# Optimization experiments

Hardware: AMD Instinct MI355X
Metric: run time of the kernel (lower is better)

The kernel has to match this reference:

```python
import jax, jax.numpy as jnp
import numpy as np

B, T, E, H, N_TAGS = 128, 512, 256, 512, 32
START, END = 30, 31


def setup_inputs() -> dict:
    key = jax.random.key(0)
    ks = jax.random.split(key, 12)
    s = 1.0 / np.sqrt(H)

    def w(k, shape):
        return jax.random.normal(k, shape, jnp.float32) * s

    X = jax.random.normal(ks[0], (B, T, E), jnp.float32)
    length = jnp.sort(jax.random.randint(ks[1], (B,), T // 2, T + 1))[::-1]
    masks = (jnp.arange(T)[None, :] < length[:, None]).astype(jnp.float32)
    W_ih_f, W_hh_f, b_f = w(ks[2], (4 * H, E)), w(ks[3], (4 * H, H)), w(ks[4], (4 * H,))
    W_ih_b, W_hh_b, b_b = w(ks[5], (4 * H, E)), w(ks[6], (4 * H, H)), w(ks[7], (4 * H,))
    W_out, b_out = w(ks[8], (N_TAGS, 2 * H)), w(ks[9], (N_TAGS,))
    transitions = jax.random.normal(ks[10], (N_TAGS, N_TAGS), jnp.float32)
    transitions = transitions.at[:, START].set(-1e4).at[END, :].set(-1e4)
    return dict(X=X, masks=masks, length=length,
                W_ih_f=W_ih_f, W_hh_f=W_hh_f, b_f=b_f,
                W_ih_b=W_ih_b, W_hh_b=W_hh_b, b_b=b_b,
                W_out=W_out, b_out=b_out, transitions=transitions)


def _lstm_dir(Xt, mt, Wih, Whh, b, reverse):
    # Xt: [T,B,E], mt: [T,B,1]. Masked update emulates pack_padded_sequence
    # (state frozen on pad; for reverse dir, state stays zero until last valid token).
    h0 = jnp.zeros((Xt.shape[1], H), Xt.dtype)

    def step(carry, inp):
        h, c = carry
        x, m = inp
        gates = x @ Wih.T + h @ Whh.T + b  # [B,4H], torch gate order i,f,g,o
        i, f, g, o = jnp.split(gates, 4, axis=-1)
        i, f, o = jax.nn.sigmoid(i), jax.nn.sigmoid(f), jax.nn.sigmoid(o)
        g = jnp.tanh(g)
        c_new = f * c + i * g
        h_new = o * jnp.tanh(c_new)
        h = m * h_new + (1.0 - m) * h
        c = m * c_new + (1.0 - m) * c
        return (h, c), h

    _, hs = jax.lax.scan(step, (h0, h0), (Xt, mt), reverse=reverse)
    return hs  # [T,B,H]


def reference(X, masks, length, W_ih_f, W_hh_f, b_f, W_ih_b, W_hh_b, b_b, W_out, b_out, transitions):
    Xt = X.transpose(1, 0, 2)            # [T,B,E]
    mT = masks.T                          # [T,B]
    mt = mT[:, :, None]
    hf = _lstm_dir(Xt, mt, W_ih_f, W_hh_f, b_f, False)
    hb = _lstm_dir(Xt, mt, W_ih_b, W_hh_b, b_b, True)
    emis = jnp.concatenate([hf, hb], axis=-1) @ W_out.T + b_out  # [T,B,n_tags]

    # Viterbi forward recurrence with masking
    alphas0 = emis[0] + transitions[START]  # [B,n]

    def vstep(alphas, inp):
        e, m = inp  # e: [B,n], m: [B,1]
        scores = alphas[:, :, None] + transitions[None] + e[:, None, :]  # [B,from,to]
        alphas = m * scores.max(axis=1) + (1.0 - m) * alphas
        return alphas, jnp.argmax(scores, axis=1)

    alphas, bps = jax.lax.scan(vstep, alphas0, (emis[1:], mt[1:]))
    final = alphas + transitions[:, END]
    max_end_scores = final.max(axis=1)      # [B]
    end_tags = jnp.argmax(final, axis=1)    # [B]

    # Masked backtrace: bps[k] is the backpointer into position k+1
    def bstep(cur, inp):
        bp, m = inp  # bp: [B,n], m: [B]
        prev = jnp.where(m > 0, jnp.take_along_axis(bp, cur[:, None], axis=1)[:, 0], cur)
        return prev, prev

    _, outs = jax.lax.scan(bstep, end_tags, (bps, mT[1:]), reverse=True)  # outs[k]=tag at pos k
    tags = jnp.concatenate([outs, end_tags[None]], axis=0).T              # [B,T]
    tags = jnp.where(masks > 0, tags, -1)
    return max_end_scores, tags
```

## Files before the change

kernel.cpp:

```cpp
#include <hip/hip_runtime.h>
#include <cfloat>
#include <cmath>

#define Bn 128
#define Tn 512
#define En 256
#define Hn 512
#define NTAGS 32
#define CHK 64
#define NCHK 12

#define OFF_HF 0
#define OFF_HB 131072
#define OFF_CF 262144
#define OFF_CB 327680
#define OFF_EF 393216
#define OFF_EB 2490368

__device__ __forceinline__ void gll16(const float* g, float* l) {
  __builtin_amdgcn_global_load_lds(
      (const __attribute__((address_space(1))) void*)g,
      (__attribute__((address_space(3))) void*)l, 16, 0, 0);
}

__global__ __launch_bounds__(512, 2) void lstm_step_k(
    const float* __restrict__ X, const float* __restrict__ masks,
    const float* __restrict__ Wih_f, const float* __restrict__ Whh_f, const float* __restrict__ bias_f,
    const float* __restrict__ Wih_b, const float* __restrict__ Whh_b, const float* __restrict__ bias_b,
    const float* __restrict__ Wout, float* __restrict__ ws, int s)
{
  __shared__ __align__(16) float WT[768 * 16];
  __shared__ __align__(16) float HX[2][CHK * Bn];
  __shared__ __align__(16) float GL[Bn * 17];
  __shared__ __align__(16) float WoL[512];
  __shared__ __align__(16) float RS[16 * 32];

  const int tid  = threadIdx.x;
  const int blk  = blockIdx.x;
  const int lane = tid & 63;
  const int wid  = __builtin_amdgcn_readfirstlane(tid >> 6);
  const int cg   = wid & 1;
  const int kt   = wid >> 1;

  const int dir = blk >> 7;
  const int bbk = blk & 127;
  const int t = dir ? (Tn - 1 - s) : s;
  const float* Wih  = dir ? Wih_b  : Wih_f;
  const float* Whh  = dir ? Whh_b  : Whh_f;
  const float* bias = dir ? bias_b : bias_f;
  float* hbuf = ws + (dir ? OFF_HB : OFF_HF);
  float* cbuf = ws + (dir ? OFF_CB : OFF_CF);
  const int rbuf = (s + 1) & 1;
  const int wbuf = s & 1;
  const float* hprev = hbuf + rbuf * (Hn * Bn);
  float*       hnext = hbuf + wbuf * (Hn * Bn);
  const int hidx0 = bbk * 4;

  const int etag = bbk & 31;
  const int ebq  = bbk >> 5;

  #pragma unroll
  for (int r = 0; r < 4; ++r) {
    const int item = r * 512 + tid;
    gll16(hprev + item * 4, &HX[0][item * 4]);
  }
  {
    const int lc  = tid & 15;
    const int q   = tid >> 4;
    const int row = (lc >> 2) * Hn + hidx0 + (lc & 3);
    #pragma unroll
    for (int i = 0; i < 6; ++i) {
      const int k4 = q + i * 32;
      const int k  = k4 * 4;
      float4 w4;
      if (k < Hn) w4 = *(const float4*)&Whh[(size_t)row * Hn + k];
      else        w4 = *(const float4*)&Wih[(size_t)row * En + (k - Hn)];
      WT[(k + 0) * 16 + lc] = w4.x; WT[(k + 1) * 16 + lc] = w4.y;
      WT[(k + 2) * 16 + lc] = w4.z; WT[(k + 3) * 16 + lc] = w4.w;
    }
  }
  if (tid < 128) {
    const float4 wo = *(const float4*)&Wout[(size_t)etag * (2 * Hn) + dir * Hn + tid * 4];
    WoL[tid * 4 + 0] = wo.x; WoL[tid * 4 + 1] = wo.y;
    WoL[tid * 4 + 2] = wo.z; WoL[tid * 4 + 3] = wo.w;
  }
  __syncthreads();

  float acc[2][8];
  #pragma unroll
  for (int m = 0; m < 2; ++m)
    #pragma unroll
    for (int n = 0; n < 8; ++n) acc[m][n] = 0.f;
  float eacc = 0.f;
  float4 xr[4];

  #pragma unroll 1
  for (int c = 0; c < NCHK; ++c) {
    const int nxt = c + 1;
    if (nxt < 8) {
      const float* src = hprev + nxt * (CHK * Bn);
      float* dst = &HX[nxt & 1][0];
      #pragma unroll
      for (int r = 0; r < 4; ++r) {
        const int item = r * 512 + tid;
        gll16(src + item * 4, dst + item * 4);
      }
    } else if (nxt < NCHK) {
      const int e0 = (nxt - 8) * 64;
      const int bq = tid & 127;
      const int eg = tid >> 7;
      #pragma unroll
      for (int r = 0; r < 4; ++r)
        xr[r] = *(const float4*)&X[(size_t)bq * (Tn * En) + (size_t)t * En + e0 + eg * 16 + r * 4];
    }

    {
      const float* HXc = &HX[c & 1][0];
      const int kgb = c * 64 + kt * 16;
      #pragma unroll
      for (int kk = 0; kk < 16; ++kk) {
        const int kl = kt * 16 + kk;
        const float2 av = *(const float2*)&HXc[kl * Bn + lane * 2];
        const float4 wa = *(const float4*)&WT[(kgb + kk) * 16 + cg * 8];
        const float4 wb = *(const float4*)&WT[(kgb + kk) * 16 + cg * 8 + 4];
        acc[0][0] += av.x * wa.x; acc[0][1] += av.x * wa.y;
        acc[0][2] += av.x * wa.z; acc[0][3] += av.x * wa.w;
        acc[0][4] += av.x * wb.x; acc[0][5] += av.x * wb.y;
        acc[0][6] += av.x * wb.z; acc[0][7] += av.x * wb.w;
        acc[1][0] += av.y * wa.x; acc[1][1] += av.y * wa.y;
        acc[1][2] += av.y * wa.z; acc[1][3] += av.y * wa.w;
        acc[1][4] += av.y * wb.x; acc[1][5] += av.y * wb.y;
        acc[1][6] += av.y * wb.z; acc[1][7] += av.y * wb.w;
      }
      if (c < 8) {
        const int be  = tid & 31;
        const int kq  = tid >> 5;
        const int eb0 = ebq * 32 + be;
        #pragma unroll
        for (int j = 0; j < 4; ++j)
          eacc += HXc[(kq * 4 + j) * Bn + eb0] * WoL[c * 64 + kq * 4 + j];
      }
    }

    if (nxt >= 8 && nxt < NCHK) {
      float* dst = &HX[nxt & 1][0];
      const int bq = tid & 127;
      const int eg = tid >> 7;
      #pragma unroll
      for (int r = 0; r < 4; ++r) {
        const int el = eg * 16 + r * 4;
        dst[(el + 0) * Bn + bq] = xr[r].x;
        dst[(el + 1) * Bn + bq] = xr[r].y;
        dst[(el + 2) * Bn + bq] = xr[r].z;
        dst[(el + 3) * Bn + bq] = xr[r].w;
      }
    }
    __syncthreads();
  }

  RS[(tid >> 5) * 32 + (tid & 31)] = eacc;
  float* P = &HX[0][0];
  #pragma unroll
  for (int n = 0; n < 8; ++n)
    *(float2*)&P[((wid * 8) + n) * Bn + lane * 2] = make_float2(acc[0][n], acc[1][n]);
  __syncthreads();
  {
    const int b  = tid & 127;
    const int ng = tid >> 7;
    #pragma unroll
    for (int cg2 = 0; cg2 < 2; ++cg2)
      #pragma unroll
      for (int nn = 0; nn < 2; ++nn) {
        const int n = ng * 2 + nn;
        float v = 0.f;
        #pragma unroll
        for (int k2 = 0; k2 < 4; ++k2)
          v += P[((k2 * 2 + cg2) * 8 + n) * Bn + b];
        GL[b * 17 + cg2 * 8 + n] = v;
      }
  }
  __syncthreads();

  {
    const int b  = tid & 127;
    const int hh = tid >> 7;
    const int hidx = hidx0 + hh;
    const float gi = GL[b * 17 + hh]      + bias[hidx];
    const float gf = GL[b * 17 + 4 + hh]  + bias[Hn + hidx];
    const float gc = GL[b * 17 + 8 + hh]  + bias[2 * Hn + hidx];
    const float go = GL[b * 17 + 12 + hh] + bias[3 * Hn + hidx];
    const float iv = 1.f / (1.f + expf(-gi));
    const float fv = 1.f / (1.f + expf(-gf));
    const float gv = tanhf(gc);
    const float ov = 1.f / (1.f + expf(-go));
    const float cold = cbuf[hidx * Bn + b];
    const float cnew = fv * cold + iv * gv;
    const float hold = hprev[hidx * Bn + b];
    const float hnew = ov * tanhf(cnew);
    const float m = masks[(size_t)b * Tn + t];
    hnext[hidx * Bn + b] = (m > 0.f) ? hnew : hold;
    cbuf[hidx * Bn + b]  = (m > 0.f) ? cnew : cold;
  }

  if (tid < 32 && s > 0) {
    const int tprev = dir ? (Tn - s) : (s - 1);
    float* Edst = ws + (dir ? OFF_EB : OFF_EF);
    float v = 0.f;
    #pragma unroll
    for (int g = 0; g < 16; ++g) v += RS[g * 32 + tid];
    Edst[(size_t)tprev * (NTAGS * Bn) + etag * Bn + ebq * 32 + tid] = v;
  }
}

__global__ __launch_bounds__(512) void emis_final_k(const float* __restrict__ Wout,
                                                    float* __restrict__ ws)
{
  __shared__ float RSf[16 * Bn];
  const int tid = threadIdx.x;
  const int dir = blockIdx.x >> 5;
  const int tag = blockIdx.x & 31;
  const float* hsrc = ws + (dir ? OFF_HB : OFF_HF) + 1 * (Hn * Bn);
  const int tprev = dir ? 0 : (Tn - 1);
  const float* wrow = Wout + (size_t)tag * (2 * Hn) + dir * Hn;
  float* Edst = ws + (dir ? OFF_EB : OFF_EF);
  const int bq = tid & 31;
  const int kg = tid >> 5;
  float4 a4 = make_float4(0.f, 0.f, 0.f, 0.f);
  #pragma unroll 4
  for (int kk = 0; kk < 32; ++kk) {
    const int k = kg * 32 + kk;
    const float w = wrow[k];
    const float4 h4 = *(const float4*)&hsrc[k * Bn + bq * 4];
    a4.x += h4.x * w; a4.y += h4.y * w; a4.z += h4.z * w; a4.w += h4.w * w;
  }
  *(float4*)&RSf[kg * Bn + bq * 4] = a4;
  __syncthreads();
  if (tid < 128) {
    float v = 0.f;
    #pragma unroll
    for (int g = 0; g < 16; ++g) v += RSf[g * Bn + tid];
    Edst[(size_t)tprev * (NTAGS * Bn) + tag * Bn + tid] = v;
  }
}

__global__ __launch_bounds__(64) void viterbi_k(
    const float* __restrict__ Ef, const float* __restrict__ Eb,
    const float* __restrict__ bout, const float* __restrict__ trans,
    const float* __restrict__ masks, float* __restrict__ out)
{
  const int b = blockIdx.x;
  const int l = threadIdx.x;
  __shared__ float tr[32][32];
  __shared__ float al[32];
  __shared__ float msk[512];
  __shared__ unsigned char bp[512][32];
  __shared__ int tseq[512];

  for (int i = l; i < 1024; i += 64) tr[i >> 5][i & 31] = trans[i];
  for (int i = l; i < 512; i += 64) msk[i] = masks[(size_t)b * 512 + i];
  __syncthreads();

  const int j  = l & 31;
  const int hi = l >> 5;
  if (l < 32)
    al[j] = Ef[(size_t)j * Bn + b] + Eb[(size_t)j * Bn + b] + bout[j] + tr[30][j];
  __syncthreads();

  for (int t = 1; t < 512; ++t) {
    float pmax = -FLT_MAX; int pidx = 0;
    #pragma unroll
    for (int ii = 0; ii < 16; ++ii) {
      const int i = hi * 16 + ii;
      const float sc = al[i] + tr[i][j];
      if (sc > pmax) { pmax = sc; pidx = i; }
    }
    const float omax = __shfl_down(pmax, 32);
    const int   oidx = __shfl_down(pidx, 32);
    if (l < 32) {
      if (omax > pmax) { pmax = omax; pidx = oidx; }
      bp[t][j] = (unsigned char)pidx;
      const float e = Ef[(size_t)t * (NTAGS * Bn) + j * Bn + b]
                    + Eb[(size_t)t * (NTAGS * Bn) + j * Bn + b] + bout[j];
      const float na = pmax + e;
      if (msk[t] > 0.f) al[j] = na;
    }
    __syncthreads();
  }

  float fv; int fidx;
  if (l < 32) { fv = al[l] + tr[l][31]; fidx = l; }
  else        { fv = -FLT_MAX; fidx = 1 << 30; }
  #pragma unroll
  for (int off = 16; off >= 1; off >>= 1) {
    const float v2 = __shfl_xor(fv, off);
    const int   i2 = __shfl_xor(fidx, off);
    if (v2 > fv || (v2 == fv && i2 < fidx)) { fv = v2; fidx = i2; }
  }
  if (l == 0) {
    out[b] = fv;
    int cur = fidx;
    tseq[511] = cur;
    for (int t = 511; t >= 1; --t) {
      const int prev = (msk[t] > 0.f) ? (int)bp[t][cur] : cur;
      tseq[t - 1] = prev;
      cur = prev;
    }
  }
  __syncthreads();
  for (int t = l; t < 512; t += 64) {
    const float tv = (msk[t] > 0.f) ? (float)tseq[t] : -1.0f;
    out[Bn + (size_t)b * 512 + t] = tv;
  }
}

extern "C" void kernel_launch(void* const* d_in, const int* in_sizes, int n_in,
                              void* d_out, int out_size, void* d_ws, size_t ws_size,
                              hipStream_t stream) {
  const float* X      = (const float*)d_in[0];
  const float* masks  = (const float*)d_in[1];
  const float* Wih_f  = (const float*)d_in[3];
  const float* Whh_f  = (const float*)d_in[4];
  const float* bf     = (const float*)d_in[5];
  const float* Wih_b  = (const float*)d_in[6];
  const float* Whh_b  = (const float*)d_in[7];
  const float* bb     = (const float*)d_in[8];
  const float* Wout   = (const float*)d_in[9];
  const float* bout   = (const float*)d_in[10];
  const float* trans  = (const float*)d_in[11];
  float* ws  = (float*)d_ws;
  float* out = (float*)d_out;

  hipMemsetAsync(d_ws, 0, (size_t)OFF_EF * sizeof(float), stream);

  for (int s = 0; s < Tn; ++s)
    lstm_step_k<<<256, 512, 0, stream>>>(X, masks, Wih_f, Whh_f, bf,
                                         Wih_b, Whh_b, bb, Wout, ws, s);
  emis_final_k<<<64, 512, 0, stream>>>(Wout, ws);
  viterbi_k<<<128, 64, 0, stream>>>(ws + OFF_EF, ws + OFF_EB, bout, trans, masks, out);
}
```

Baseline: 12.23 ms.

## Widen per-thread LSTM GEMM tile to 4x8 with padded LDS and register staging

Each thread now computes 4 batch rows by 8 gate columns per k, with the k-split across the two half-waves. This raises arithmetic intensity per LDS load. The async global-to-LDS copies are replaced by register-staged float4 loads written into LDS with a padded row stride (LDW=132, WPAD=20) to cut bank conflicts. The cross-warp partial-sum reduction is reorganised to sum 8 k-slices. In exchange, register pressure rises and the direct async LDS loads are lost, which could limit occupancy under launch_bounds(512,2).

```diff
diff --git a/kernel.cpp b/kernel.cpp
--- a/kernel.cpp
+++ b/kernel.cpp
@@ -9,6 +9,8 @@
 #define NTAGS 32
 #define CHK 64
 #define NCHK 12
+#define LDW 132
+#define WPAD 20
 
 #define OFF_HF 0
 #define OFF_HB 131072
@@ -17,30 +19,26 @@
 #define OFF_EF 393216
 #define OFF_EB 2490368
 
-__device__ __forceinline__ void gll16(const float* g, float* l) {
-  __builtin_amdgcn_global_load_lds(
-      (const __attribute__((address_space(1))) void*)g,
-      (__attribute__((address_space(3))) void*)l, 16, 0, 0);
-}
-
 __global__ __launch_bounds__(512, 2) void lstm_step_k(
     const float* __restrict__ X, const float* __restrict__ masks,
     const float* __restrict__ Wih_f, const float* __restrict__ Whh_f, const float* __restrict__ bias_f,
     const float* __restrict__ Wih_b, const float* __restrict__ Whh_b, const float* __restrict__ bias_b,
     const float* __restrict__ Wout, float* __restrict__ ws, int s)
 {
-  __shared__ __align__(16) float WT[768 * 16];
-  __shared__ __align__(16) float HX[2][CHK * Bn];
+  __shared__ __align__(16) float WT[768 * WPAD];
+  __shared__ __align__(16) float HX[2][CHK * LDW];
   __shared__ __align__(16) float GL[Bn * 17];
   __shared__ __align__(16) float WoL[512];
   __shared__ __align__(16) float RS[16 * 32];
 
-  const int tid  = threadIdx.x;
-  const int blk  = blockIdx.x;
-  const int lane = tid & 63;
-  const int wid  = __builtin_amdgcn_readfirstlane(tid >> 6);
-  const int cg   = wid & 1;
-  const int kt   = wid >> 1;
+  const int tid   = threadIdx.x;
+  const int blk   = blockIdx.x;
+  const int lane  = tid & 63;
+  const int wid   = __builtin_amdgcn_readfirstlane(tid >> 6);
+  const int cg    = wid & 1;
+  const int kt    = wid >> 1;
+  const int bg    = lane & 31;
+  const int khalf = lane >> 5;
 
   const int dir = blk >> 7;
   const int bbk = blk & 127;
@@ -59,125 +57,130 @@
   const int etag = bbk & 31;
   const int ebq  = bbk >> 5;
 
-  #pragma unroll
-  for (int r = 0; r < 4; ++r) {
-    const int item = r * 512 + tid;
-    gll16(hprev + item * 4, &HX[0][item * 4]);
-  }
   {
-    const int lc  = tid & 15;
-    const int q   = tid >> 4;
+    const int lc = tid & 15;
+    const int kw = tid >> 4;
     const int row = (lc >> 2) * Hn + hidx0 + (lc & 3);
     #pragma unroll
     for (int i = 0; i < 6; ++i) {
-      const int k4 = q + i * 32;
-      const int k  = k4 * 4;
+      const int k = (kw + i * 32) * 4;
       float4 w4;
       if (k < Hn) w4 = *(const float4*)&Whh[(size_t)row * Hn + k];
       else        w4 = *(const float4*)&Wih[(size_t)row * En + (k - Hn)];
-      WT[(k + 0) * 16 + lc] = w4.x; WT[(k + 1) * 16 + lc] = w4.y;
-      WT[(k + 2) * 16 + lc] = w4.z; WT[(k + 3) * 16 + lc] = w4.w;
+      WT[(k + 0) * WPAD + lc] = w4.x; WT[(k + 1) * WPAD + lc] = w4.y;
+      WT[(k + 2) * WPAD + lc] = w4.z; WT[(k + 3) * WPAD + lc] = w4.w;
     }
   }
   if (tid < 128) {
     const float4 wo = *(const float4*)&Wout[(size_t)etag * (2 * Hn) + dir * Hn + tid * 4];
-    WoL[tid * 4 + 0] = wo.x; WoL[tid * 4 + 1] = wo.y;
-    WoL[tid * 4 + 2] = wo.z; WoL[tid * 4 + 3] = wo.w;
-  }
-  __syncthreads();
-
-  float acc[2][8];
+    *(float4*)&WoL[tid * 4] = wo;
+  }
+  {
+    #pragma unroll
+    for (int r = 0; r < 4; ++r) {
+      const int item = r * 512 + tid;
+      const float4 v = *(const float4*)&hprev[item * 4];
+      const int k = item >> 5;
+      const int g = item & 31;
+      *(float4*)&HX[0][k * LDW + g * 4] = v;
+    }
+  }
+  __syncthreads();
+
+  float acc[4][8];
   #pragma unroll
-  for (int m = 0; m < 2; ++m)
+  for (int m = 0; m < 4; ++m)
     #pragma unroll
     for (int n = 0; n < 8; ++n) acc[m][n] = 0.f;
   float eacc = 0.f;
-  float4 xr[4];
+
+  const int xbq = tid & 127;
+  const int xeg = tid >> 7;
 
   #pragma unroll 1
   for (int c = 0; c < NCHK; ++c) {
     const int nxt = c + 1;
+    float4 st[4];
     if (nxt < 8) {
       const float* src = hprev + nxt * (CHK * Bn);
+      #pragma unroll
+      for (int r = 0; r < 4; ++r)
+        st[r] = *(const float4*)&src[(r * 512 + tid) * 4];
+    } else if (nxt < NCHK) {
+      const int e0 = (nxt - 8) * CHK;
+      #pragma unroll
+      for (int r = 0; r < 4; ++r)
+        st[r] = *(const float4*)&X[(size_t)xbq * (Tn * En) + (size_t)t * En + e0 + xeg * 16 + r * 4];
+    }
+
+    {
+      const float* HXc = &HX[c & 1][0];
+      #pragma unroll
+      for (int j = 0; j < 8; ++j) {
+        const int l = kt * 16 + j * 2 + khalf;
+        const float4 av = *(const float4*)&HXc[l * LDW + bg * 4];
+        const float4 wa = *(const float4*)&WT[(c * 64 + l) * WPAD + cg * 8];
+        const float4 wb = *(const float4*)&WT[(c * 64 + l) * WPAD + cg * 8 + 4];
+        const float avf[4] = {av.x, av.y, av.z, av.w};
+        const float wvf[8] = {wa.x, wa.y, wa.z, wa.w, wb.x, wb.y, wb.z, wb.w};
+        #pragma unroll
+        for (int m = 0; m < 4; ++m)
+          #pragma unroll
+          for (int n = 0; n < 8; ++n)
+            acc[m][n] += avf[m] * wvf[n];
+      }
+      if (c < 8) {
+        const int be = tid & 31;
+        const int kq = tid >> 5;
+        #pragma unroll
+        for (int j = 0; j < 4; ++j)
+          eacc += HXc[(kq * 4 + j) * LDW + ebq * 32 + be] * WoL[c * 64 + kq * 4 + j];
+      }
+    }
+
+    if (nxt < 8) {
       float* dst = &HX[nxt & 1][0];
       #pragma unroll
       for (int r = 0; r < 4; ++r) {
         const int item = r * 512 + tid;
-        gll16(src + item * 4, dst + item * 4);
+        const int k = item >> 5;
+        const int g = item & 31;
+        *(float4*)&dst[k * LDW + g * 4] = st[r];
       }
     } else if (nxt < NCHK) {
-      const int e0 = (nxt - 8) * 64;
-      const int bq = tid & 127;
-      const int eg = tid >> 7;
-      #pragma unroll
-      for (int r = 0; r < 4; ++r)
-        xr[r] = *(const float4*)&X[(size_t)bq * (Tn * En) + (size_t)t * En + e0 + eg * 16 + r * 4];
-    }
-
-    {
-      const float* HXc = &HX[c & 1][0];
-      const int kgb = c * 64 + kt * 16;
-      #pragma unroll
-      for (int kk = 0; kk < 16; ++kk) {
-        const int kl = kt * 16 + kk;
-        const float2 av = *(const float2*)&HXc[kl * Bn + lane * 2];
-        const float4 wa = *(const float4*)&WT[(kgb + kk) * 16 + cg * 8];
-        const float4 wb = *(const float4*)&WT[(kgb + kk) * 16 + cg * 8 + 4];
-        acc[0][0] += av.x * wa.x; acc[0][1] += av.x * wa.y;
-        acc[0][2] += av.x * wa.z; acc[0][3] += av.x * wa.w;
-        acc[0][4] += av.x * wb.x; acc[0][5] += av.x * wb.y;
-        acc[0][6] += av.x * wb.z; acc[0][7] += av.x * wb.w;
-        acc[1][0] += av.y * wa.x; acc[1][1] += av.y * wa.y;
-        acc[1][2] += av.y * wa.z; acc[1][3] += av.y * wa.w;
-        acc[1][4] += av.y * wb.x; acc[1][5] += av.y * wb.y;
-        acc[1][6] += av.y * wb.z; acc[1][7] += av.y * wb.w;
+      float* dst = &HX[nxt & 1][0];
+      #pragma unroll
+      for (int r = 0; r < 4; ++r) {
+        const int el = xeg * 16 + r * 4;
+        dst[(el + 0) * LDW + xbq] = st[r].x;
+        dst[(el + 1) * LDW + xbq] = st[r].y;
+        dst[(el + 2) * LDW + xbq] = st[r].z;
+        dst[(el + 3) * LDW + xbq] = st[r].w;
       }
-      if (c < 8) {
-        const int be  = tid & 31;
-        const int kq  = tid >> 5;
-        const int eb0 = ebq * 32 + be;
-        #pragma unroll
-        for (int j = 0; j < 4; ++j)
-          eacc += HXc[(kq * 4 + j) * Bn + eb0] * WoL[c * 64 + kq * 4 + j];
-      }
-    }
-
-    if (nxt >= 8 && nxt < NCHK) {
-      float* dst = &HX[nxt & 1][0];
-      const int bq = tid & 127;
-      const int eg = tid >> 7;
-      #pragma unroll
-      for (int r = 0; r < 4; ++r) {
-        const int el = eg * 16 + r * 4;
-        dst[(el + 0) * Bn + bq] = xr[r].x;
-        dst[(el + 1) * Bn + bq] = xr[r].y;
-        dst[(el + 2) * Bn + bq] = xr[r].z;
-        dst[(el + 3) * Bn + bq] = xr[r].w;
-      }
     }
     __syncthreads();
   }
 
-  RS[(tid >> 5) * 32 + (tid & 31)] = eacc;
   float* P = &HX[0][0];
+  const int ks = kt * 2 + khalf;
   #pragma unroll
   for (int n = 0; n < 8; ++n)
-    *(float2*)&P[((wid * 8) + n) * Bn + lane * 2] = make_float2(acc[0][n], acc[1][n]);
+    *(float4*)&P[ks * 2048 + (cg * 8 + n) * 128 + bg * 4] =
+        make_float4(acc[0][n], acc[1][n], acc[2][n], acc[3][n]);
+  RS[(tid >> 5) * 32 + (tid & 31)] = eacc;
   __syncthreads();
   {
     const int b  = tid & 127;
-    const int ng = tid >> 7;
-    #pragma unroll
-    for (int cg2 = 0; cg2 < 2; ++cg2)
-      #pragma unroll
-      for (int nn = 0; nn < 2; ++nn) {
-        const int n = ng * 2 + nn;
-        float v = 0.f;
-        #pragma unroll
-        for (int k2 = 0; k2 < 4; ++k2)
-          v += P[((k2 * 2 + cg2) * 8 + n) * Bn + b];
-        GL[b * 17 + cg2 * 8 + n] = v;
-      }
+    const int cq = tid >> 7;
+    float g4[4] = {0.f, 0.f, 0.f, 0.f};
+    #pragma unroll
+    for (int k2 = 0; k2 < 8; ++k2)
+      #pragma unroll
+      for (int ci = 0; ci < 4; ++ci)
+        g4[ci] += P[k2 * 2048 + (cq * 4 + ci) * 128 + b];
+    #pragma unroll
+    for (int ci = 0; ci < 4; ++ci)
+      GL[b * 17 + cq * 4 + ci] = g4[ci];
   }
   __syncthreads();
 
```

Measured after the change: 11.37 ms. -7.1%, faster.
